# Optimization experiments

Hardware: AMD Instinct MI355X
Metric: run time of the kernel (lower is better)

Reference implementation:

```python
import jax, jax.numpy as jnp
import numpy as np

N, C_IN, C_K, C_V, H = 8192, 512, 512, 512, 8


def setup_inputs() -> dict:
    key = jax.random.key(0)
    ks = jax.random.split(key, 9)
    s = 0.02
    return {
        "input_": jax.random.normal(ks[0], (N, C_IN), dtype=jnp.float32),
        "Wk": jax.random.normal(ks[1], (C_IN, C_K), dtype=jnp.float32) * s,
        "bk": jnp.zeros((C_K,), dtype=jnp.float32),
        "Wq": jax.random.normal(ks[2], (C_IN, C_K), dtype=jnp.float32) * s,
        "bq": jnp.zeros((C_K,), dtype=jnp.float32),
        "Wv": jax.random.normal(ks[3], (C_IN, C_V), dtype=jnp.float32) * s,
        "bv": jnp.zeros((C_V,), dtype=jnp.float32),
        "Wr": jax.random.normal(ks[4], (C_K, C_K), dtype=jnp.float32) * s,
        "br": jnp.zeros((C_K,), dtype=jnp.float32),
    }


def reference(input_, Wk, bk, Wq, bq, Wv, bv, Wr, br):
    n = input_.shape[0]
    keys = input_ @ Wk + bk      # [N, C_K]
    queries = input_ @ Wq + bq   # [N, C_K]
    values = input_ @ Wv + bv    # [N, C_V]
    hk = C_K // H
    hv = C_V // H
    # [H, N, hk] / [H, N, hv]
    k = keys.reshape(n, H, hk).transpose(1, 0, 2)
    q = queries.reshape(n, H, hk).transpose(1, 0, 2)
    v = values.reshape(n, H, hv).transpose(1, 0, 2)
    k_sm = jax.nn.softmax(k, axis=1)   # softmax over tokens (dim=0 in torch)
    q_sm = jax.nn.softmax(q, axis=2)   # softmax over head channels (dim=1)
    # context = key^T @ value per head: [H, hk, hv]
    context = jnp.einsum('hnk,hnv->hkv', k_sm, v)
    attended = jnp.einsum('hnk,hkv->hnv', q_sm, context)  # [H, N, hv]
    # concat heads along channel dim -> [N, C_V]
    aggregated = attended.transpose(1, 0, 2).reshape(n, C_V)
    attention = aggregated @ Wr + br
    # mean over heads of q_sm @ k_sm^T; contracting h and k jointly = one GEMM
    scores = jnp.einsum('hnk,hmk->nm', q_sm, k_sm) / H  # [N, N]
    return attention, scores
```

## Files before the change

### kernel.cpp

```cpp
#include <hip/hip_runtime.h>

#define NT 8192
#define CD 512
#define NH 8
#define SC_N 8192

using f32x4  = __attribute__((ext_vector_type(4))) float;
using bf16x8 = __attribute__((ext_vector_type(8))) __bf16;

__device__ __forceinline__ unsigned short f2bf(float x) {
    union { float f; unsigned u; } c; c.f = x;
    unsigned r = c.u + 0x7fffu + ((c.u >> 16) & 1u);
    return (unsigned short)(r >> 16);
}
__device__ __forceinline__ float bf2f(unsigned short b) {
    union { float f; unsigned u; } c; c.u = ((unsigned)b) << 16;
    return c.f;
}

__global__ void prep_k(const float4* __restrict__ in, unsigned short* __restrict__ out,
                       const float* __restrict__ Wk, const float* __restrict__ Wq,
                       const float* __restrict__ Wv, const float* __restrict__ bk,
                       const float* __restrict__ bq, const float* __restrict__ bv,
                       unsigned short* __restrict__ Wt, float* __restrict__ biaskqv) {
    int b = blockIdx.x;
    if (b < 4096) {
        int i = b * 256 + threadIdx.x;
        float4 v = in[i];
        out[i*4+0] = f2bf(v.x);
        out[i*4+1] = f2bf(v.y);
        out[i*4+2] = f2bf(v.z);
        out[i*4+3] = f2bf(v.w);
    } else {
        int idx = (b - 4096) * 256 + threadIdx.x;
        int c = idx >> 9, k = idx & 511;
        int sec = c >> 9, cc = c & 511;
        const float* W = (sec == 0) ? Wk : ((sec == 1) ? Wq : Wv);
        Wt[idx] = f2bf(W[k * 512 + cc]);
        if (idx < 1536) {
            const float* bb = (idx < 512) ? bk : ((idx < 1024) ? bq : bv);
            biaskqv[idx] = bb[idx & 511];
        }
    }
}

__global__ __launch_bounds__(256) void kqv_gemm_k(
    const unsigned short* __restrict__ A, const unsigned short* __restrict__ Bt,
    const float* __restrict__ bias,
    unsigned short* __restrict__ kbf, unsigned short* __restrict__ qsm,
    unsigned short* __restrict__ vbf,
    float* __restrict__ pmax, float* __restrict__ psum)
{
    __shared__ unsigned short sA[128 * 32];
    __shared__ unsigned short sB[128 * 32];
    const int tid  = threadIdx.x;
    const int wid  = tid >> 6;
    const int lane = tid & 63;
    const int col0 = blockIdx.x * 128;
    const int row0 = blockIdx.y * 128;
    const int by   = blockIdx.y;
    const int wr = (wid >> 1) * 64;
    const int wc = (wid & 1) * 64;
    const int fr = lane & 15;
    const int fq = lane >> 4;
    const int srow = lane >> 2;
    const int scol = (lane & 3) * 8;

    f32x4 acc[4][4] = {};

    for (int kt = 0; kt < 16; ++kt) {
        const int k0 = kt << 5;
        __syncthreads();
        #pragma unroll
        for (int s = 0; s < 2; ++s) {
            const int seg = wid * 2 + s;
            const unsigned short* gA = A + (size_t)(row0 + seg * 16 + srow) * 512 + k0 + scol;
            __builtin_amdgcn_global_load_lds(
                (const __attribute__((address_space(1))) void*)gA,
                (__attribute__((address_space(3))) void*)(sA + seg * 512), 16, 0, 0);
            const unsigned short* gB = Bt + (size_t)(col0 + seg * 16 + srow) * 512 + k0 + scol;
            __builtin_amdgcn_global_load_lds(
                (const __attribute__((address_space(1))) void*)gB,
                (__attribute__((address_space(3))) void*)(sB + seg * 512), 16, 0, 0);
        }
        __syncthreads();

        bf16x8 av[4], bfrag[4];
        #pragma unroll
        for (int m = 0; m < 4; ++m)
            av[m] = *(const bf16x8*)(sA + (wr + m * 16 + fr) * 32 + fq * 8);
        #pragma unroll
        for (int n = 0; n < 4; ++n)
            bfrag[n] = *(const bf16x8*)(sB + (wc + n * 16 + fr) * 32 + fq * 8);
        #pragma unroll
        for (int m = 0; m < 4; ++m)
            #pragma unroll
            for (int n = 0; n < 4; ++n)
                acc[m][n] = __builtin_amdgcn_mfma_f32_16x16x32_bf16(av[m], bfrag[n], acc[m][n], 0, 0, 0);
    }

    const int sec = col0 >> 9;
    const int cs0 = (col0 & 511) + wc;

    if (sec == 0) {
        const int pb = by * 2 + (wr >> 6);
        #pragma unroll
        for (int n = 0; n < 4; ++n) {
            const int col = cs0 + n * 16 + fr;
            const float bv = bias[col];
            float vv[4][4], mx = -1e30f;
            #pragma unroll
            for (int m = 0; m < 4; ++m)
                #pragma unroll
                for (int r = 0; r < 4; ++r) {
                    float x = bf2f(f2bf(acc[m][n][r] + bv));
                    vv[m][r] = x; mx = fmaxf(mx, x);
                }
            mx = fmaxf(mx, __shfl_xor(mx, 16));
            mx = fmaxf(mx, __shfl_xor(mx, 32));
            float s = 0.f;
            #pragma unroll
            for (int m = 0; m < 4; ++m)
                #pragma unroll
                for (int r = 0; r < 4; ++r) {
                    s += __expf(vv[m][r] - mx);
                    kbf[(size_t)(row0 + wr + m * 16 + fq * 4 + r) * 512 + col] = f2bf(vv[m][r]);
                }
            s += __shfl_xor(s, 16);
            s += __shfl_xor(s, 32);
            if (lane < 16) { pmax[pb * 512 + col] = mx; psum[pb * 512 + col] = s; }
        }
    } else if (sec == 1) {
        #pragma unroll
        for (int m = 0; m < 4; ++m)
            #pragma unroll
            for (int r = 0; r < 4; ++r) {
                float e[4], mx = -1e30f;
                #pragma unroll
                for (int n = 0; n < 4; ++n) {
                    float x = bf2f(f2bf(acc[m][n][r] + bias[512 + cs0 + n * 16 + fr]));
                    e[n] = x; mx = fmaxf(mx, x);
                }
                mx = fmaxf(mx, __shfl_xor(mx, 1));
                mx = fmaxf(mx, __shfl_xor(mx, 2));
                mx = fmaxf(mx, __shfl_xor(mx, 4));
                mx = fmaxf(mx, __shfl_xor(mx, 8));
                float s = 0.f;
                #pragma unroll
                for (int n = 0; n < 4; ++n) { e[n] = __expf(e[n] - mx); s += e[n]; }
                s += __shfl_xor(s, 1);
                s += __shfl_xor(s, 2);
                s += __shfl_xor(s, 4);
                s += __shfl_xor(s, 8);
                const float rs = 1.f / s;
                const int row = row0 + wr + m * 16 + fq * 4 + r;
                #pragma unroll
                for (int n = 0; n < 4; ++n)
                    qsm[(size_t)row * 512 + cs0 + n * 16 + fr] = f2bf(e[n] * rs);
            }
    } else {
        #pragma unroll
        for (int n = 0; n < 4; ++n) {
            const int col = cs0 + n * 16 + fr;
            const float bv = bias[1024 + col];
            #pragma unroll
            for (int m = 0; m < 4; ++m)
                #pragma unroll
                for (int r = 0; r < 4; ++r)
                    vbf[(size_t)(row0 + wr + m * 16 + fq * 4 + r) * 512 + col] = f2bf(acc[m][n][r] + bv);
        }
    }
}

__global__ __launch_bounds__(256) void ksmctx_k(
    const unsigned short* __restrict__ kbf, const unsigned short* __restrict__ vbf,
    const float* __restrict__ pmax, const float* __restrict__ psum,
    unsigned short* __restrict__ ksm, float* __restrict__ pctx)
{
    const int ch = blockIdx.x;
    const int h  = blockIdx.y;
    const int tid = threadIdx.x, w = tid >> 6, lane = tid & 63;
    const int fr = lane & 15, fq = lane >> 4;
    __shared__ unsigned short tr[4][2][4096];
    __shared__ float redm[4][64], reds[4][64], cmx[64], crc[64];

    {
        const int c = tid & 63, q = tid >> 6;
        const int col = h * 64 + c;
        float m = -1e30f;
        for (int r = 0; r < 32; ++r) m = fmaxf(m, pmax[(q * 32 + r) * 512 + col]);
        float s = 0.f;
        for (int r = 0; r < 32; ++r)
            s += psum[(q * 32 + r) * 512 + col] * __expf(pmax[(q * 32 + r) * 512 + col] - m);
        redm[q][c] = m; reds[q][c] = s;
    }
    __syncthreads();
    if (tid < 64) {
        float m = fmaxf(fmaxf(redm[0][tid], redm[1][tid]), fmaxf(redm[2][tid], redm[3][tid]));
        float s = 0.f;
        #pragma unroll
        for (int q = 0; q < 4; ++q) s += reds[q][tid] * __expf(redm[q][tid] - m);
        cmx[tid] = m; crc[tid] = 1.f / s;
    }
    __syncthreads();

    char* kt = (char*)&tr[w][0][0];
    char* vt = (char*)&tr[w][1][0];
    const int nbase = ch * 256 + w * 64;
    #pragma unroll
    for (int j = 0; j < 8; ++j) {
        bf16x8 kv = *(const bf16x8*)(kbf + (size_t)(nbase + lane) * 512 + h * 64 + j * 8);
        bf16x8 vv = *(const bf16x8*)(vbf + (size_t)(nbase + lane) * 512 + h * 64 + j * 8);
        unsigned short ko[8];
        #pragma unroll
        for (int e = 0; e < 8; ++e) {
            int k = j * 8 + e;
            float x = __expf(bf2f(((const unsigned short*)&kv)[e]) - cmx[k]) * crc[k];
            unsigned short us = f2bf(x);
            ko[e] = us;
            int byte = (k * 128 + lane * 2) ^ (e << 4);
            *(unsigned short*)(kt + byte) = us;
            *(unsigned short*)(vt + byte) = ((const unsigned short*)&vv)[e];
        }
        *(uint4*)(ksm + (size_t)(nbase + lane) * 512 + h * 64 + j * 8) = *(const uint4*)ko;
    }
    asm volatile("s_waitcnt lgkmcnt(0)" ::: "memory");
    __builtin_amdgcn_sched_barrier(0);

    f32x4 acc[4][4] = {};
    #pragma unroll
    for (int ks = 0; ks < 2; ++ks) {
        bf16x8 a[4], b[4];
        #pragma unroll
        for (int mf = 0; mf < 4; ++mf) {
            int row  = mf * 16 + fr;
            int byte = (row * 128 + (ks * 4 + fq) * 16) ^ ((row & 7) << 4);
            a[mf] = *(const bf16x8*)(kt + byte);
            b[mf] = *(const bf16x8*)(vt + byte);
        }
        #pragma unroll
        for (int mf = 0; mf < 4; ++mf)
            #pragma unroll
            for (int nf = 0; nf < 4; ++nf)
                acc[mf][nf] = __builtin_amdgcn_mfma_f32_16x16x32_bf16(a[mf], b[nf], acc[mf][nf], 0, 0, 0);
    }

    float* red = (float*)&tr[w][0][0];
    #pragma unroll
    for (int mf = 0; mf < 4; ++mf)
        #pragma unroll
        for (int nf = 0; nf < 4; ++nf)
            #pragma unroll
            for (int r = 0; r < 4; ++r) {
                int lr = mf * 16 + fq * 4 + r;
                int lc = (nf * 16 + fr) ^ (((lr >> 2) & 1) << 4);
                red[lr * 64 + lc] = acc[mf][nf][r];
            }
    __syncthreads();
    const float* rbase = (const float*)&tr[0][0][0];
    float* out = pctx + (size_t)(ch * 8 + h) * 4096;
    #pragma unroll
    for (int it = 0; it < 16; ++it) {
        int e = it * 256 + tid;
        int lr = e >> 6;
        int ph = (lr * 64) + ((e & 63) ^ (((lr >> 2) & 1) << 4));
        float s = rbase[ph] + rbase[4096 + ph] + rbase[8192 + ph] + rbase[12288 + ph];
        out[e] = s;
    }
}

__global__ void mtred_k(const float* __restrict__ pctx, const float* __restrict__ Wr,
                        unsigned short* __restrict__ Mt) {
    __shared__ float cr[64];
    const int b = blockIdx.x;
    const int hk = b >> 1;
    const int o  = (b & 1) * 256 + threadIdx.x;
    const int h = hk >> 6, k = hk & 63;
    if (threadIdx.x < 64) {
        float s = 0.f;
        for (int p = 0; p < 32; ++p)
            s += pctx[(size_t)(p * 8 + h) * 4096 + k * 64 + threadIdx.x];
        cr[threadIdx.x] = s;
    }
    __syncthreads();
    const float* wp = Wr + (size_t)(h * 64) * 512 + o;
    float s = 0.f;
    #pragma unroll
    for (int j = 0; j < 64; ++j)
        s += cr[j] * wp[(size_t)j * 512];
    Mt[(size_t)o * 512 + hk] = f2bf(s);
}

__global__ __launch_bounds__(256, 3) void scores_attn_k(
    const unsigned short* __restrict__ qsm, const unsigned short* __restrict__ ksm,
    const unsigned short* __restrict__ Mt, const float* __restrict__ br,
    float* __restrict__ attn_out, float* __restrict__ scores_out)
{
    __shared__ unsigned short sA0[128 * 32], sA1[128 * 32];
    __shared__ unsigned short sB0[128 * 32], sB1[128 * 32];
    const int tid  = threadIdx.x;
    const int wid  = tid >> 6;
    const int lane = tid & 63;
    const int wr = (wid >> 1) * 64;
    const int wc = (wid & 1) * 64;
    const int fr = lane & 15;
    const int fq = lane >> 4;
    const int srow = lane >> 2;
    const int scol = (lane & 3) * 8;

    const bool is_attn = blockIdx.x < 256;
    int row0, col0;
    const unsigned short* Bt;
    if (is_attn) {
        const int bx = blockIdx.x;
        col0 = (bx & 3) * 128;
        row0 = (bx >> 2) * 128;
        Bt = Mt;
    } else {
        int g = blockIdx.x - 256;
        g = (g & 7) * 512 + (g >> 3);
        row0 = ((g & 7) + ((g >> 9) << 3)) * 128;
        col0 = ((g >> 3) & 63) * 128;
        Bt = ksm;
    }

    f32x4 acc[4][4] = {};

    auto STAGE = [&](int kt, unsigned short* dA, unsigned short* dB) {
        const int k0 = kt << 5;
        #pragma unroll
        for (int s = 0; s < 2; ++s) {
            const int seg = wid * 2 + s;
            const unsigned short* gA = qsm + (size_t)(row0 + seg * 16 + srow) * 512 + k0 + scol;
            __builtin_amdgcn_global_load_lds(
                (const __attribute__((address_space(1))) void*)gA,
                (__attribute__((address_space(3))) void*)(dA + seg * 512), 16, 0, 0);
            const unsigned short* gB = Bt + (size_t)(col0 + seg * 16 + srow) * 512 + k0 + scol;
            __builtin_amdgcn_global_load_lds(
                (const __attribute__((address_space(1))) void*)gB,
                (__attribute__((address_space(3))) void*)(dB + seg * 512), 16, 0, 0);
        }
    };

    auto BODY = [&](int kt, const unsigned short* cA, const unsigned short* cB,
                    unsigned short* nA, unsigned short* nB) {
        if (kt < 15) STAGE(kt + 1, nA, nB);
        __builtin_amdgcn_sched_barrier(0);
        bf16x8 av[4], bfrag[4];
        #pragma unroll
        for (int m = 0; m < 4; ++m)
            av[m] = *(const bf16x8*)(cA + (wr + m * 16 + fr) * 32 + fq * 8);
        #pragma unroll
        for (int n = 0; n < 4; ++n)
            bfrag[n] = *(const bf16x8*)(cB + (wc + n * 16 + fr) * 32 + fq * 8);
        __builtin_amdgcn_s_setprio(1);
        #pragma unroll
        for (int m = 0; m < 4; ++m)
            #pragma unroll
            for (int n = 0; n < 4; ++n)
                acc[m][n] = __builtin_amdgcn_mfma_f32_16x16x32_bf16(av[m], bfrag[n], acc[m][n], 0, 0, 0);
        __builtin_amdgcn_s_setprio(0);
        asm volatile("s_waitcnt vmcnt(0)" ::: "memory");
        __builtin_amdgcn_s_barrier();
        __builtin_amdgcn_sched_barrier(0);
    };

    STAGE(0, sA0, sB0);
    asm volatile("s_waitcnt vmcnt(0)" ::: "memory");
    __builtin_amdgcn_s_barrier();
    __builtin_amdgcn_sched_barrier(0);

    #pragma unroll
    for (int kt = 0; kt < 16; kt += 2) {
        BODY(kt,     sA0, sB0, sA1, sB1);
        BODY(kt + 1, sA1, sB1, sA0, sB0);
    }

    if (is_attn) {
        #pragma unroll
        for (int n = 0; n < 4; ++n) {
            const int col = col0 + wc + n * 16 + fr;
            const float bval = br[col];
            #pragma unroll
            for (int m = 0; m < 4; ++m) {
                #pragma unroll
                for (int r = 0; r < 4; ++r) {
                    const int row = row0 + wr + m * 16 + fq * 4 + r;
                    __builtin_nontemporal_store(acc[m][n][r] + bval, &attn_out[(size_t)row * 512 + col]);
                }
            }
        }
    } else {
        #pragma unroll
        for (int n = 0; n < 4; ++n) {
            const int col = col0 + wc + n * 16 + fr;
            #pragma unroll
            for (int m = 0; m < 4; ++m) {
                #pragma unroll
                for (int r = 0; r < 4; ++r) {
                    const int row = row0 + wr + m * 16 + fq * 4 + r;
                    __builtin_nontemporal_store(acc[m][n][r] * 0.125f, &scores_out[(size_t)row * SC_N + col]);
                }
            }
        }
    }
}

extern "C" void kernel_launch(void* const* d_in, const int* in_sizes, int n_in,
                              void* d_out, int out_size, void* d_ws, size_t ws_size,
                              hipStream_t stream) {
    const float* input = (const float*)d_in[0];
    const float* Wk = (const float*)d_in[1];
    const float* bk = (const float*)d_in[2];
    const float* Wq = (const float*)d_in[3];
    const float* bq = (const float*)d_in[4];
    const float* Wv = (const float*)d_in[5];
    const float* bv = (const float*)d_in[6];
    const float* Wr = (const float*)d_in[7];
    const float* br = (const float*)d_in[8];

    char* ws = (char*)d_ws;
    unsigned short* inp_bf = (unsigned short*)ws;  ws += (size_t)NT * CD * 2;
    unsigned short* Wt     = (unsigned short*)ws;  ws += (size_t)1536 * 512 * 2;
    float* biaskqv         = (float*)ws;           ws += 1536 * 4;
    unsigned short* kbf    = (unsigned short*)ws;  ws += (size_t)NT * CD * 2;
    unsigned short* qsm    = (unsigned short*)ws;  ws += (size_t)NT * CD * 2;
    unsigned short* vbf    = (unsigned short*)ws;  ws += (size_t)NT * CD * 2;
    unsigned short* ksm    = (unsigned short*)ws;  ws += (size_t)NT * CD * 2;
    float* pmax            = (float*)ws;           ws += 128 * 512 * 4;
    float* psum            = (float*)ws;           ws += 128 * 512 * 4;
    float* pctx            = (float*)ws;           ws += (size_t)32 * 8 * 4096 * 4;
    unsigned short* Mt     = (unsigned short*)ws;  ws += (size_t)512 * 512 * 2;

    float* attn_out   = (float*)d_out;
    float* scores_out = (float*)d_out + (size_t)NT * CD;

    prep_k<<<7168, 256, 0, stream>>>((const float4*)input, inp_bf,
                                     Wk, Wq, Wv, bk, bq, bv, Wt, biaskqv);

    kqv_gemm_k<<<dim3(12, 64), 256, 0, stream>>>(inp_bf, Wt, biaskqv,
                                                 kbf, qsm, vbf, pmax, psum);

    ksmctx_k<<<dim3(32, 8), 256, 0, stream>>>(kbf, vbf, pmax, psum, ksm, pctx);

    mtred_k<<<1024, 256, 0, stream>>>(pctx, Wr, Mt);

    scores_attn_k<<<4352, 256, 0, stream>>>(qsm, ksm, Mt, br, attn_out, scores_out);
}
```

Measured before the change: 168.2 us.

## Fold Mt reduction into scores kernel with atomic counter dependency

Merges the separate mtred kernel into the scores/attention kernel as its first 1024 blocks. Attention blocks spin-wait on a global atomic counter until all Mt blocks have finished, while the score blocks run without waiting. This removes one kernel launch and its drain gap, and lets the large scores GEMM overlap the small Mt work. It relies on lower block indices being scheduled first to avoid deadlock, and it adds spin-wait overhead. The counter is reset in prep_k.

```diff
diff --git a/kernel.cpp b/kernel.cpp
--- a/kernel.cpp
+++ b/kernel.cpp
@@ -22,8 +22,10 @@
                        const float* __restrict__ Wk, const float* __restrict__ Wq,
                        const float* __restrict__ Wv, const float* __restrict__ bk,
                        const float* __restrict__ bq, const float* __restrict__ bv,
-                       unsigned short* __restrict__ Wt, float* __restrict__ biaskqv) {
+                       unsigned short* __restrict__ Wt, float* __restrict__ biaskqv,
+                       int* __restrict__ cnt) {
     int b = blockIdx.x;
+    if (b == 0 && threadIdx.x == 0) *cnt = 0;
     if (b < 4096) {
         int i = b * 256 + threadIdx.x;
         float4 v = in[i];
@@ -269,36 +271,42 @@
     }
 }
 
-__global__ void mtred_k(const float* __restrict__ pctx, const float* __restrict__ Wr,
-                        unsigned short* __restrict__ Mt) {
-    __shared__ float cr[64];
-    const int b = blockIdx.x;
-    const int hk = b >> 1;
-    const int o  = (b & 1) * 256 + threadIdx.x;
-    const int h = hk >> 6, k = hk & 63;
-    if (threadIdx.x < 64) {
-        float s = 0.f;
-        for (int p = 0; p < 32; ++p)
-            s += pctx[(size_t)(p * 8 + h) * 4096 + k * 64 + threadIdx.x];
-        cr[threadIdx.x] = s;
-    }
-    __syncthreads();
-    const float* wp = Wr + (size_t)(h * 64) * 512 + o;
-    float s = 0.f;
-    #pragma unroll
-    for (int j = 0; j < 64; ++j)
-        s += cr[j] * wp[(size_t)j * 512];
-    Mt[(size_t)o * 512 + hk] = f2bf(s);
-}
-
 __global__ __launch_bounds__(256, 3) void scores_attn_k(
     const unsigned short* __restrict__ qsm, const unsigned short* __restrict__ ksm,
-    const unsigned short* __restrict__ Mt, const float* __restrict__ br,
-    float* __restrict__ attn_out, float* __restrict__ scores_out)
+    const float* __restrict__ pctx, const float* __restrict__ Wr,
+    unsigned short* __restrict__ Mt, const float* __restrict__ br,
+    float* __restrict__ attn_out, float* __restrict__ scores_out,
+    int* __restrict__ cnt)
 {
     __shared__ unsigned short sA0[128 * 32], sA1[128 * 32];
     __shared__ unsigned short sB0[128 * 32], sB1[128 * 32];
     const int tid  = threadIdx.x;
+
+    if (blockIdx.x < 1024) {
+        float* cr = (float*)sA0;
+        const int b = blockIdx.x;
+        const int hk = b >> 1;
+        const int o  = (b & 1) * 256 + tid;
+        const int h = hk >> 6, k = hk & 63;
+        if (tid < 64) {
+            float s = 0.f;
+            for (int p = 0; p < 32; ++p)
+                s += pctx[(size_t)(p * 8 + h) * 4096 + k * 64 + tid];
+            cr[tid] = s;
+        }
+        __syncthreads();
+        const float* wp = Wr + (size_t)(h * 64) * 512 + o;
+        float s = 0.f;
+        #pragma unroll
+        for (int j = 0; j < 64; ++j)
+            s += cr[j] * wp[(size_t)j * 512];
+        Mt[(size_t)o * 512 + hk] = f2bf(s);
+        __threadfence();
+        __syncthreads();
+        if (tid == 0) atomicAdd(cnt, 1);
+        return;
+    }
+
     const int wid  = tid >> 6;
     const int lane = tid & 63;
     const int wr = (wid >> 1) * 64;
@@ -308,16 +316,19 @@
     const int srow = lane >> 2;
     const int scol = (lane & 3) * 8;
 
-    const bool is_attn = blockIdx.x < 256;
+    const bool is_attn = blockIdx.x < 1280;
     int row0, col0;
     const unsigned short* Bt;
     if (is_attn) {
-        const int bx = blockIdx.x;
+        if (tid == 0) { while (atomicAdd(cnt, 0) < 1024) __builtin_amdgcn_s_sleep(8); }
+        __syncthreads();
+        __threadfence();
+        const int bx = blockIdx.x - 1024;
         col0 = (bx & 3) * 128;
         row0 = (bx >> 2) * 128;
         Bt = Mt;
     } else {
-        int g = blockIdx.x - 256;
+        int g = blockIdx.x - 1280;
         g = (g & 7) * 512 + (g >> 3);
         row0 = ((g & 7) + ((g >> 9) << 3)) * 128;
         col0 = ((g >> 3) & 63) * 128;
@@ -431,19 +442,19 @@
     float* psum            = (float*)ws;           ws += 128 * 512 * 4;
     float* pctx            = (float*)ws;           ws += (size_t)32 * 8 * 4096 * 4;
     unsigned short* Mt     = (unsigned short*)ws;  ws += (size_t)512 * 512 * 2;
+    int* cnt               = (int*)ws;             ws += 128;
 
     float* attn_out   = (float*)d_out;
     float* scores_out = (float*)d_out + (size_t)NT * CD;
 
     prep_k<<<7168, 256, 0, stream>>>((const float4*)input, inp_bf,
-                                     Wk, Wq, Wv, bk, bq, bv, Wt, biaskqv);
+                                     Wk, Wq, Wv, bk, bq, bv, Wt, biaskqv, cnt);
 
     kqv_gemm_k<<<dim3(12, 64), 256, 0, stream>>>(inp_bf, Wt, biaskqv,
                                                  kbf, qsm, vbf, pmax, psum);
 
     ksmctx_k<<<dim3(32, 8), 256, 0, stream>>>(kbf, vbf, pmax, psum, ksm, pctx);
 
-    mtred_k<<<1024, 256, 0, stream>>>(pctx, Wr, Mt);
-
-    scores_attn_k<<<4352, 256, 0, stream>>>(qsm, ksm, Mt, br, attn_out, scores_out);
-}
+    scores_attn_k<<<5376, 256, 0, stream>>>(qsm, ksm, pctx, Wr, Mt, br,
+                                            attn_out, scores_out, cnt);
+}
```

Result: slower. 328.6 us (+95.4%).
